# Kernel optimization log

Hardware: AMD Instinct MI355X
Metric: run time of the kernel (lower is better)

Reference implementation:

```python
import jax, jax.numpy as jnp
import numpy as np

N_STEPS = 5
STATE_DIM = 512
ANN_DIM = 256
N_NODES = 2048
N_EDGE_TYPES = 4


def setup_inputs() -> dict:
    key = jax.random.key(0)
    ks = jax.random.split(key, 12)
    D, E, N = STATE_DIM, N_EDGE_TYPES, N_NODES
    s = 0.02
    adjacency = (jax.random.uniform(ks[0], (N, N * 2 * E)) < 0.015).astype(jnp.float32)
    annotations = jax.random.normal(ks[1], (N, ANN_DIM), dtype=jnp.float32)
    W_prop = jax.random.normal(ks[2], (2 * E, D, D), dtype=jnp.float32) * s
    b_prop = jnp.zeros((2 * E, D), dtype=jnp.float32)
    Wz = jax.random.normal(ks[3], (D, D), dtype=jnp.float32) * s
    Uz = jax.random.normal(ks[4], (D, D), dtype=jnp.float32) * s
    bz = jnp.zeros((D,), dtype=jnp.float32)
    Wr = jax.random.normal(ks[5], (D, D), dtype=jnp.float32) * s
    Ur = jax.random.normal(ks[6], (D, D), dtype=jnp.float32) * s
    br = jnp.zeros((D,), dtype=jnp.float32)
    Wh = jax.random.normal(ks[7], (D, D), dtype=jnp.float32) * s
    Uh = jax.random.normal(ks[8], (D, D), dtype=jnp.float32) * s
    bh = jnp.zeros((D,), dtype=jnp.float32)
    return dict(adjacency=adjacency, annotations=annotations, W_prop=W_prop, b_prop=b_prop,
                Wz=Wz, Uz=Uz, bz=bz, Wr=Wr, Ur=Ur, br=br, Wh=Wh, Uh=Uh, bh=bh)


def reference(adjacency, annotations, W_prop, b_prop, Wz, Uz, bz, Wr, Ur, br, Wh, Uh, bh):
    N = annotations.shape[0]
    D = W_prop.shape[-1]
    # pad annotations into first columns of state (input1[:, :ann_dim] = annotations)
    h = jnp.zeros((N, D), dtype=annotations.dtype).at[:, :annotations.shape[1]].set(annotations)
    for _ in range(N_STEPS):
        # per-edge-type linear transforms: edge_type_list [2E, N, D]
        t = jnp.einsum('nd,edf->enf', h, W_prop) + b_prop[:, None, :]
        # adjacency aggregation: A is [N, N*2E] with per-edge-type column blocks
        a = adjacency @ t.reshape(-1, D)  # [N, D]
        # GRU node update (UpdateNet)
        z = jax.nn.sigmoid(a @ Wz + h @ Uz + bz)
        r = jax.nn.sigmoid(a @ Wr + h @ Ur + br)
        h_tilde = jnp.tanh(a @ Wh + (r * h) @ Uh + bh)
        h = (1.0 - z) * h + z * h_tilde
    return h
```

## Files before the change

### kernel.cpp

```cpp
#include <hip/hip_runtime.h>

typedef __attribute__((ext_vector_type(8))) short short8;
typedef __attribute__((ext_vector_type(4))) float floatx4;
typedef __attribute__((ext_vector_type(2))) unsigned uintx2;

#define NSTEPS 5
#define DD 512
#define ANN 256
#define NNODE 2048
#define NEDGE 8
#define NCOLS (NNODE * NEDGE)
#define MAXE 96
#define KP (NEDGE * DD)


typedef __attribute__((address_space(3))) unsigned lds_u32;
typedef const __attribute__((address_space(1))) unsigned g_u32;
__device__ __forceinline__ void gload16(const short* g, short* l) {
    __builtin_amdgcn_global_load_lds((g_u32*)g, (lds_u32*)l, 16, 0, 0);
}

__device__ inline float bf2f(unsigned short s) {
    unsigned u = ((unsigned)s) << 16;
    float f; __builtin_memcpy(&f, &u, 4);
    return f;
}
__device__ inline unsigned short f2bf(float f) {
    unsigned u; __builtin_memcpy(&u, &f, 4);
    u += 0x7fffu + ((u >> 16) & 1u);
    return (unsigned short)(u >> 16);
}
__device__ inline void split2(float x, unsigned short& hi, unsigned short& lo) {
    hi = f2bf(x);
    lo = f2bf(x - bf2f(hi));
}
__device__ inline void fo_write(short* __restrict__ Fhi, short* __restrict__ Flo,
                                int row, int col, float v) {
    unsigned short hs, ls;
    split2(v, hs, ls);
    size_t a = ((size_t)(row >> 4) * 64 + (col >> 3)) * 128 + ((row & 15) << 3) + (col & 7);
    Fhi[a] = (short)hs;
    Flo[a] = (short)ls;
}
__device__ inline void fo_write2(short* __restrict__ Fhi, short* __restrict__ Flo,
                                 int row, int c, float v0, float v1) {
    unsigned short h0, l0, h1, l1;
    split2(v0, h0, l0);
    split2(v1, h1, l1);
    size_t a = ((size_t)(row >> 4) * 64 + (c >> 3)) * 128 + ((row & 15) << 3) + (c & 7);
    *(unsigned*)(Fhi + a) = (unsigned)h0 | ((unsigned)h1 << 16);
    *(unsigned*)(Flo + a) = (unsigned)l0 | ((unsigned)l1 << 16);
}

__global__ __launch_bounds__(256) void k_init(const float* __restrict__ ann,
                                              float* __restrict__ h,
                                              short* __restrict__ HBhi,
                                              short* __restrict__ HBlo,
                                              int* __restrict__ cnt2,
                                              unsigned short* __restrict__ idx) {
    int n = blockIdx.x, t = threadIdx.x;
    int c = 2 * t;
    float v0 = 0.f, v1 = 0.f;
    if (c < ANN) {
        v0 = ann[(size_t)n * ANN + c];
        v1 = ann[(size_t)n * ANN + c + 1];
    }
    h[(size_t)n * DD + c]     = v0;
    h[(size_t)n * DD + c + 1] = v1;
    fo_write2(HBhi, HBlo, n, c, v0, v1);
    if (t < NEDGE) cnt2[n * NEDGE + t] = 0;
    unsigned* ip = (unsigned*)(idx + (size_t)n * NEDGE * MAXE);
    for (int j = t; j < NEDGE * MAXE / 2; j += 256)
        ip[j] = 2048u | (2048u << 16);
    if (n == 0) {
        h[(size_t)NNODE * DD + c]     = 0.f;
        h[(size_t)NNODE * DD + c + 1] = 0.f;
    }
}

__global__ __launch_bounds__(256) void k_build(const float* __restrict__ adj,
                                               int* __restrict__ cnt2,
                                               unsigned short* __restrict__ idx) {
    int n = blockIdx.x;
    const float* row = adj + (size_t)n * NCOLS;
    for (int j8 = threadIdx.x; j8 < NCOLS / 8; j8 += 256) {
        floatx4 a = *(const floatx4*)(row + j8 * 8);
        floatx4 b = *(const floatx4*)(row + j8 * 8 + 4);
        unsigned nz = 0;
        #pragma unroll
        for (int i = 0; i < 4; i++) {
            if (a[i] != 0.f) nz |= 1u << i;
            if (b[i] != 0.f) nz |= 1u << (4 + i);
        }
        while (nz) {
            int i = __builtin_ctz(nz);
            nz &= nz - 1;
            int j = j8 * 8 + i;
            int e = j >> 11;
            int m = j & (NNODE - 1);
            int p = atomicAdd(&cnt2[n * NEDGE + e], 1);
            if (p < MAXE) idx[((size_t)n * NEDGE + e) * MAXE + p] = (unsigned short)m;
        }
    }
}

__global__ __launch_bounds__(256) void k_transP(const float* __restrict__ W,
                                                short* __restrict__ Fhi,
                                                short* __restrict__ Flo, int K) {
    __shared__ float st[32][33];
    int tx = threadIdx.x & 31, ty = threadIdx.x >> 5;
    int k0 = blockIdx.x * 32, n0 = blockIdx.y * 32;
    #pragma unroll
    for (int i = 0; i < 4; i++)
        st[ty + i * 8][tx] = W[(size_t)(k0 + ty + i * 8) * DD + n0 + tx];
    __syncthreads();
    #pragma unroll
    for (int i = 0; i < 4; i++) {
        int n = n0 + ty + i * 8, k = k0 + tx;
        float v = st[tx][ty + i * 8];
        unsigned short hs, ls;
        split2(v, hs, ls);
        size_t a = ((size_t)(n >> 4) * (K >> 3) + (k >> 3)) * 128 + ((n & 15) << 3) + (k & 7);
        Fhi[a] = (short)hs;
        Flo[a] = (short)ls;
    }
}

__global__ __launch_bounds__(256) void k_transG(const float* __restrict__ s00,
                                                const float* __restrict__ s10,
                                                const float* __restrict__ s01,
                                                const float* __restrict__ s11,
                                                short* __restrict__ Fhi,
                                                short* __restrict__ Flo) {
    __shared__ float st[32][33];
    const int K = 2 * DD;
    int tx = threadIdx.x & 31, ty = threadIdx.x >> 5;
    int k0 = blockIdx.x * 32, n0 = blockIdx.y * 32;
    const float* sk0 = (n0 < DD) ? s00 : s01;
    const float* sk1 = (n0 < DD) ? s10 : s11;
    #pragma unroll
    for (int i = 0; i < 4; i++) {
        int k = k0 + ty + i * 8;
        const float* s = (k < DD) ? sk0 : sk1;
        st[ty + i * 8][tx] = s[(size_t)(k & (DD - 1)) * DD + ((n0 + tx) & (DD - 1))];
    }
    __syncthreads();
    #pragma unroll
    for (int i = 0; i < 4; i++) {
        int n = n0 + ty + i * 8, k = k0 + tx;
        float v = st[tx][ty + i * 8];
        unsigned short hs, ls;
        split2(v, hs, ls);
        size_t a = ((size_t)(n >> 4) * (K >> 3) + (k >> 3)) * 128 + ((n & 15) << 3) + (k & 7);
        Fhi[a] = (short)hs;
        Flo[a] = (short)ls;
    }
}

__global__ __launch_bounds__(256) void k_gather_all(const float* __restrict__ h,
                                                    const int* __restrict__ cnt2,
                                                    const unsigned short* __restrict__ idx,
                                                    short* __restrict__ Gbhi,
                                                    short* __restrict__ Gblo) {
    __shared__ unsigned short sidx[8 * MAXE];
    __shared__ int scnt[8];
    const int bid = blockIdx.x;
    const int ep = bid & 3;
    const int g  = bid >> 2;
    const int n0 = g * 4;
    const int t  = threadIdx.x;
    const int dn = t >> 6;
    const int th2 = t & 63;

    if (t < 8) scnt[t] = cnt2[(n0 + (t >> 1)) * NEDGE + 2 * ep + (t & 1)];
    {
        const unsigned* src0 = (const unsigned*)(idx + ((size_t)n0 * NEDGE + 2 * ep) * MAXE);
        for (int j = t; j < 384; j += 256) {
            int d = j / 96;
            int w = j - d * 96;
            ((unsigned*)sidx)[d * 96 + w] = src0[(size_t)d * (NEDGE * MAXE / 2) + w];
        }
    }
    __syncthreads();

    const float* hp = h + 8 * th2;

    floatx4 e0c0, e0c1, e1c0, e1c1;
    auto gather_edge = [&](int le, floatx4& o0, floatx4& o1) {
        int m = scnt[dn * 2 + le];
        m = m > MAXE ? MAXE : m;
        m = (m + 3) & ~3;
        const unsigned short* row = &sidx[dn * 192 + le * 96];
        floatx4 a0 = (floatx4){0.f, 0.f, 0.f, 0.f};
        floatx4 a1 = (floatx4){0.f, 0.f, 0.f, 0.f};
        floatx4 b0 = (floatx4){0.f, 0.f, 0.f, 0.f};
        floatx4 b1 = (floatx4){0.f, 0.f, 0.f, 0.f};
        for (int i = 0; i < m; i += 4) {
            uintx2 w = *(const uintx2*)(row + i);
            const float* r0 = hp + (size_t)(w[0] & 0xffffu) * DD;
            const float* r1 = hp + (size_t)(w[0] >> 16) * DD;
            const float* r2 = hp + (size_t)(w[1] & 0xffffu) * DD;
            const float* r3 = hp + (size_t)(w[1] >> 16) * DD;
            floatx4 v0 = *(const floatx4*)r0;
            floatx4 v1 = *(const floatx4*)(r0 + 4);
            floatx4 v2 = *(const floatx4*)r1;
            floatx4 v3 = *(const floatx4*)(r1 + 4);
            floatx4 v4 = *(const floatx4*)r2;
            floatx4 v5 = *(const floatx4*)(r2 + 4);
            floatx4 v6 = *(const floatx4*)r3;
            floatx4 v7 = *(const floatx4*)(r3 + 4);
            a0 += v0; a1 += v1; b0 += v2; b1 += v3;
            a0 += v4; a1 += v5; b0 += v6; b1 += v7;
        }
        o0 = a0 + b0;
        o1 = a1 + b1;
    };
    gather_edge(0, e0c0, e0c1);
    gather_edge(1, e1c0, e1c1);

    __syncthreads();

    #pragma unroll
    for (int le = 0; le < 2; le++) {
        floatx4 c0 = le ? e1c0 : e0c0;
        floatx4 c1 = le ? e1c1 : e0c1;
        int ge = 2 * ep + le;
        unsigned short hs[8], ls[8];
        #pragma unroll
        for (int j = 0; j < 4; j++) {
            split2(c0[j], hs[j], ls[j]);
            split2(c1[j], hs[4 + j], ls[4 + j]);
        }
        short8 hv, lv;
        #pragma unroll
        for (int j = 0; j < 8; j++) { hv[j] = (short)hs[j]; lv[j] = (short)ls[j]; }
        size_t a = ((size_t)(n0 >> 4) * 512 + ge * 64 + th2) * 128
                 + (size_t)((n0 & 15) + dn) * 8;
        *(short8*)(Gbhi + a) = hv;
        *(short8*)(Gblo + a) = lv;
    }
}

template<int MODE>
__global__ __launch_bounds__(256, 4) void k_gemm8(
    const short* __restrict__ A0hi, const short* __restrict__ A0lo,
    const short* __restrict__ A1hi, const short* __restrict__ A1lo,
    const short* __restrict__ Bhi,  const short* __restrict__ Blo,
    const float* __restrict__ bias0, const float* __restrict__ bias1,
    float* __restrict__ zbuf,
    float* __restrict__ h,
    short* __restrict__ Ohi, short* __restrict__ Olo,
    float* __restrict__ P0, float* __restrict__ P1) {

    __shared__ short S[24][512];

    const int tid = threadIdx.x;
    const int lane = tid & 63;
    const int wave = tid >> 6;
    const int wm = wave >> 1;
    const int wn = wave & 1;
    const int quad = lane >> 4;
    const int l16 = lane & 15;

    const int pbid = blockIdx.x;
    const int x = pbid & 7;
    const int j = pbid >> 3;
    const int mband = x * 4 + (j & 3);
    int kh, bx;
    if (MODE == 1) { kh = 0; bx = j >> 2; }
    else           { kh = (j >> 2) & 1; bx = j >> 3; }
    const int blockM = mband * 64;
    const int blockN = bx * 32;
    const int mt0 = blockM >> 4, nt0 = blockN >> 4;
    const int KCB = (MODE == 0) ? 512 : 128;
    const int bko = (MODE == 0) ? kh * 256 : (MODE == 2 ? kh * 64 : 0);
    const int Kloc = (MODE == 0) ? 2048 : (MODE == 1 ? 1024 : 512);

    const short* Ahi_s = (MODE == 2 && kh) ? A1hi : A0hi;
    const short* Alo_s = (MODE == 2 && kh) ? A1lo : A0lo;

    floatx4 acc[2];
    acc[0] = (floatx4){0.f, 0.f, 0.f, 0.f};
    acc[1] = (floatx4){0.f, 0.f, 0.f, 0.f};

    auto gaddr = [&](int k0, int s) -> const short* {
        if (s < 16) {
            int pl = s >> 3, u = s & 7;
            int mt = u >> 1, ks = u & 1;
            const short* base;
            int kc, stride;
            if (MODE == 0) {
                base = pl ? A0lo : A0hi;
                kc = kh * 256 + (k0 >> 3) + ks * 4;
                stride = 512;
            } else if (MODE == 1) {
                int seg = k0 >> 9;
                base = seg ? (pl ? A1lo : A1hi) : (pl ? A0lo : A0hi);
                kc = ((k0 & 511) >> 3) + ks * 4;
                stride = 64;
            } else {
                base = pl ? Alo_s : Ahi_s;
                kc = (k0 >> 3) + ks * 4;
                stride = 64;
            }
            return base + ((size_t)(mt0 + mt) * stride + kc) * 128;
        } else {
            int u = s - 16, pl = u >> 2, ks = (u >> 1) & 1, nt = u & 1;
            const short* base = pl ? Blo : Bhi;
            return base + ((size_t)(nt0 + nt) * KCB + bko + (k0 >> 3) + ks * 4) * 128;
        }
    };

    for (int k0 = 0; k0 < Kloc; k0 += 64) {
        #pragma unroll
        for (int jj = 0; jj < 6; jj++) {
            int s = jj * 4 + wave;
            gload16(gaddr(k0, s) + lane * 8, &S[s][lane * 8]);
        }
        __syncthreads();

        #pragma unroll
        for (int ks = 0; ks < 2; ks++) {
            short8 ah[2], al[2], bh, bl;
            #pragma unroll
            for (int mi = 0; mi < 2; mi++) {
                ah[mi] = *(const short8*)&S[(wm * 2 + mi) * 2 + ks][lane * 8];
                al[mi] = *(const short8*)&S[8 + (wm * 2 + mi) * 2 + ks][lane * 8];
            }
            bh = *(const short8*)&S[16 + ks * 2 + wn][lane * 8];
            bl = *(const short8*)&S[20 + ks * 2 + wn][lane * 8];
            #pragma unroll
            for (int mi = 0; mi < 2; mi++) {
                acc[mi] = __builtin_amdgcn_mfma_f32_16x16x32_bf16(ah[mi], bh, acc[mi], 0, 0, 0);
                acc[mi] = __builtin_amdgcn_mfma_f32_16x16x32_bf16(ah[mi], bl, acc[mi], 0, 0, 0);
                acc[mi] = __builtin_amdgcn_mfma_f32_16x16x32_bf16(al[mi], bh, acc[mi], 0, 0, 0);
            }
        }
        __syncthreads();
    }

    float* P = kh ? P1 : P0;
    #pragma unroll
    for (int mi = 0; mi < 2; mi++) {
        int gcol = blockN + wn * 16 + l16;
        #pragma unroll
        for (int r = 0; r < 4; r++) {
            int grow = blockM + wm * 32 + mi * 16 + quad * 4 + r;
            float v = acc[mi][r];
            if (MODE == 0 || MODE == 2) {
                P[(size_t)grow * DD + gcol] = v;
            } else {
                if (gcol < DD) {
                    size_t o = (size_t)grow * DD + gcol;
                    zbuf[o] = 1.f / (1.f + __expf(-(v + bias0[gcol])));
                } else {
                    int c = gcol - DD;
                    size_t o = (size_t)grow * DD + c;
                    float rr = 1.f / (1.f + __expf(-(v + bias1[c])));
                    fo_write(Ohi, Olo, grow, c, rr * h[o]);
                }
            }
        }
    }
}

__global__ __launch_bounds__(256) void k_combP(const float* __restrict__ P0,
                                               const float* __restrict__ P1,
                                               const int* __restrict__ cnt2,
                                               const float* __restrict__ bp,
                                               short* __restrict__ Gahi,
                                               short* __restrict__ Galo) {
    int n = blockIdx.x, t = threadIdx.x;
    int c = 2 * t;
    float s0 = 0.f, s1 = 0.f;
    #pragma unroll
    for (int e = 0; e < NEDGE; e++) {
        float ce = (float)cnt2[n * NEDGE + e];
        s0 += ce * bp[e * DD + c];
        s1 += ce * bp[e * DD + c + 1];
    }
    size_t o = (size_t)n * DD + c;
    float v0 = P0[o] + P1[o] + s0;
    float v1 = P0[o + 1] + P1[o + 1] + s1;
    fo_write2(Gahi, Galo, n, c, v0, v1);
}

__global__ __launch_bounds__(256) void k_combF(const float* __restrict__ P0,
                                               const float* __restrict__ P1,
                                               const float* __restrict__ bh,
                                               const float* __restrict__ zbuf,
                                               float* __restrict__ h,
                                               short* __restrict__ HBhi,
                                               short* __restrict__ HBlo,
                                               float* __restrict__ outF) {
    int n = blockIdx.x, t = threadIdx.x;
    int c = 2 * t;
    size_t o = (size_t)n * DD + c;
    float hn0, hn1;
    {
        float v = P0[o] + P1[o] + bh[c];
        hn0 = (1.f - zbuf[o]) * h[o] + zbuf[o] * tanhf(v);
    }
    {
        float v = P0[o + 1] + P1[o + 1] + bh[c + 1];
        hn1 = (1.f - zbuf[o + 1]) * h[o + 1] + zbuf[o + 1] * tanhf(v);
    }
    h[o] = hn0;
    h[o + 1] = hn1;
    fo_write2(HBhi, HBlo, n, c, hn0, hn1);
    outF[o] = hn0;
    outF[o + 1] = hn1;
}

extern "C" void kernel_launch(void* const* d_in, const int* in_sizes, int n_in,
                              void* d_out, int out_size, void* d_ws, size_t ws_size,
                              hipStream_t stream) {
    const float* adj = (const float*)d_in[0];
    const float* ann = (const float*)d_in[1];
    const float* Wp  = (const float*)d_in[2];
    const float* bp  = (const float*)d_in[3];
    const float* Wz  = (const float*)d_in[4];
    const float* Uz  = (const float*)d_in[5];
    const float* bz  = (const float*)d_in[6];
    const float* Wr  = (const float*)d_in[7];
    const float* Ur  = (const float*)d_in[8];
    const float* br  = (const float*)d_in[9];
    const float* Wh  = (const float*)d_in[10];
    const float* Uh  = (const float*)d_in[11];
    const float* bh  = (const float*)d_in[12];

    char* p = (char*)d_ws;
    float* h     = (float*)p; p += (size_t)(NNODE + 1) * DD * 4;
    float* abuf  = (float*)p; p += (size_t)NNODE * DD * 4;
    float* P0    = (float*)p; p += (size_t)NNODE * DD * 4;
    float* P1    = (float*)p; p += (size_t)NNODE * DD * 4;
    short* Gbhi  = (short*)p; p += (size_t)NNODE * KP * 2;
    short* Gblo  = (short*)p; p += (size_t)NNODE * KP * 2;
    short* Gahi  = (short*)p; p += (size_t)NNODE * DD * 2;
    short* Galo  = (short*)p; p += (size_t)NNODE * DD * 2;
    short* HBhi  = (short*)p; p += (size_t)NNODE * DD * 2;
    short* HBlo  = (short*)p; p += (size_t)NNODE * DD * 2;
    short* RHhi  = (short*)p; p += (size_t)NNODE * DD * 2;
    short* RHlo  = (short*)p; p += (size_t)NNODE * DD * 2;
    short* WpThi = (short*)p; p += (size_t)DD * KP * 2;
    short* WpTlo = (short*)p; p += (size_t)DD * KP * 2;
    short* ZRhi  = (short*)p; p += (size_t)(2 * DD) * (2 * DD) * 2;
    short* ZRlo  = (short*)p; p += (size_t)(2 * DD) * (2 * DD) * 2;
    short* HThi  = (short*)p; p += (size_t)DD * (2 * DD) * 2;
    short* HTlo  = (short*)p; p += (size_t)DD * (2 * DD) * 2;
    unsigned short* idx = (unsigned short*)p;
    p += (size_t)NNODE * NEDGE * MAXE * 2;
    int* cnt2 = (int*)p; p += (size_t)NNODE * NEDGE * 4;

    float* outF = (float*)d_out;

    k_init<<<NNODE, 256, 0, stream>>>(ann, h, HBhi, HBlo, cnt2, idx);
    k_build<<<NNODE, 256, 0, stream>>>(adj, cnt2, idx);
    k_transP<<<dim3(KP / 32, DD / 32), 256, 0, stream>>>(Wp, WpThi, WpTlo, KP);
    k_transG<<<dim3(32, 32), 256, 0, stream>>>(Wz, Uz, Wr, Ur, ZRhi, ZRlo);
    k_transG<<<dim3(32, 16), 256, 0, stream>>>(Wh, Uh, Wh, Uh, HThi, HTlo);

    for (int s = 0; s < NSTEPS; s++) {
        k_gather_all<<<2048, 256, 0, stream>>>(h, cnt2, idx, Gbhi, Gblo);
        k_gemm8<0><<<1024, 256, 0, stream>>>(Gbhi, Gblo, nullptr, nullptr,
                                             WpThi, WpTlo, nullptr, nullptr,
                                             nullptr, nullptr, nullptr, nullptr, P0, P1);
        k_combP<<<NNODE, 256, 0, stream>>>(P0, P1, cnt2, bp, Gahi, Galo);
        k_gemm8<1><<<1024, 256, 0, stream>>>(Gahi, Galo, HBhi, HBlo,
                                             ZRhi, ZRlo, bz, br,
                                             abuf, h, RHhi, RHlo, nullptr, nullptr);
        k_gemm8<2><<<1024, 256, 0, stream>>>(Gahi, Galo, RHhi, RHlo,
                                             HThi, HTlo, nullptr, nullptr,
                                             nullptr, nullptr, nullptr, nullptr, P0, P1);
        k_combF<<<NNODE, 256, 0, stream>>>(P0, P1, bh, abuf, h, HBhi, HBlo, outF);
    }
}
```

Baseline: 906.8 us.

## Widen GEMM tiles to 64x64 and use four-way split-K for propagation GEMM

```diff
diff --git a/kernel.cpp b/kernel.cpp
--- a/kernel.cpp
+++ b/kernel.cpp
@@ -12,6 +12,7 @@
 #define NCOLS (NNODE * NEDGE)
 #define MAXE 96
 #define KP (NEDGE * DD)
+#define NND (NNODE * DD)
 
 
 typedef __attribute__((address_space(3))) unsigned lds_u32;
@@ -250,9 +251,9 @@
     float* __restrict__ zbuf,
     float* __restrict__ h,
     short* __restrict__ Ohi, short* __restrict__ Olo,
-    float* __restrict__ P0, float* __restrict__ P1) {
-
-    __shared__ short S[24][512];
+    float* __restrict__ Pb) {
+
+    __shared__ short S[32][512];
 
     const int tid = threadIdx.x;
     const int lane = tid & 63;
@@ -267,21 +268,25 @@
     const int j = pbid >> 3;
     const int mband = x * 4 + (j & 3);
     int kh, bx;
-    if (MODE == 1) { kh = 0; bx = j >> 2; }
-    else           { kh = (j >> 2) & 1; bx = j >> 3; }
+    if (MODE == 0)      { bx = (j >> 2) & 7; kh = j >> 5; }
+    else if (MODE == 1) { bx = j >> 2;       kh = 0;      }
+    else                { kh = (j >> 2) & 1; bx = j >> 3; }
     const int blockM = mband * 64;
-    const int blockN = bx * 32;
+    const int blockN = bx * 64;
     const int mt0 = blockM >> 4, nt0 = blockN >> 4;
     const int KCB = (MODE == 0) ? 512 : 128;
-    const int bko = (MODE == 0) ? kh * 256 : (MODE == 2 ? kh * 64 : 0);
-    const int Kloc = (MODE == 0) ? 2048 : (MODE == 1 ? 1024 : 512);
+    const int bko = (MODE == 0) ? kh * 128 : (MODE == 2 ? kh * 64 : 0);
+    const int Kloc = (MODE == 2) ? 512 : 1024;
 
     const short* Ahi_s = (MODE == 2 && kh) ? A1hi : A0hi;
     const short* Alo_s = (MODE == 2 && kh) ? A1lo : A0lo;
 
-    floatx4 acc[2];
-    acc[0] = (floatx4){0.f, 0.f, 0.f, 0.f};
-    acc[1] = (floatx4){0.f, 0.f, 0.f, 0.f};
+    floatx4 acc[2][2];
+    #pragma unroll
+    for (int mi = 0; mi < 2; mi++)
+        #pragma unroll
+        for (int ni = 0; ni < 2; ni++)
+            acc[mi][ni] = (floatx4){0.f, 0.f, 0.f, 0.f};
 
     auto gaddr = [&](int k0, int s) -> const short* {
         if (s < 16) {
@@ -291,7 +296,7 @@
             int kc, stride;
             if (MODE == 0) {
                 base = pl ? A0lo : A0hi;
-                kc = kh * 256 + (k0 >> 3) + ks * 4;
+                kc = kh * 128 + (k0 >> 3) + ks * 4;
                 stride = 512;
             } else if (MODE == 1) {
                 int seg = k0 >> 9;
@@ -305,7 +310,7 @@
             }
             return base + ((size_t)(mt0 + mt) * stride + kc) * 128;
         } else {
-            int u = s - 16, pl = u >> 2, ks = (u >> 1) & 1, nt = u & 1;
+            int u = s - 16, pl = u >> 3, nt = (u & 7) >> 1, ks = u & 1;
             const short* base = pl ? Blo : Bhi;
             return base + ((size_t)(nt0 + nt) * KCB + bko + (k0 >> 3) + ks * 4) * 128;
         }
@@ -313,7 +318,7 @@
 
     for (int k0 = 0; k0 < Kloc; k0 += 64) {
         #pragma unroll
-        for (int jj = 0; jj < 6; jj++) {
+        for (int jj = 0; jj < 8; jj++) {
             int s = jj * 4 + wave;
             gload16(gaddr(k0, s) + lane * 8, &S[s][lane * 8]);
         }
@@ -321,51 +326,58 @@
 
         #pragma unroll
         for (int ks = 0; ks < 2; ks++) {
-            short8 ah[2], al[2], bh, bl;
+            short8 ah[2], al[2], bh[2], bl[2];
             #pragma unroll
             for (int mi = 0; mi < 2; mi++) {
                 ah[mi] = *(const short8*)&S[(wm * 2 + mi) * 2 + ks][lane * 8];
                 al[mi] = *(const short8*)&S[8 + (wm * 2 + mi) * 2 + ks][lane * 8];
             }
-            bh = *(const short8*)&S[16 + ks * 2 + wn][lane * 8];
-            bl = *(const short8*)&S[20 + ks * 2 + wn][lane * 8];
             #pragma unroll
-            for (int mi = 0; mi < 2; mi++) {
-                acc[mi] = __builtin_amdgcn_mfma_f32_16x16x32_bf16(ah[mi], bh, acc[mi], 0, 0, 0);
-                acc[mi] = __builtin_amdgcn_mfma_f32_16x16x32_bf16(ah[mi], bl, acc[mi], 0, 0, 0);
-                acc[mi] = __builtin_amdgcn_mfma_f32_16x16x32_bf16(al[mi], bh, acc[mi], 0, 0, 0);
+            for (int ni = 0; ni < 2; ni++) {
+                bh[ni] = *(const short8*)&S[16 + (wn * 2 + ni) * 2 + ks][lane * 8];
+                bl[ni] = *(const short8*)&S[24 + (wn * 2 + ni) * 2 + ks][lane * 8];
             }
+            #pragma unroll
+            for (int mi = 0; mi < 2; mi++)
+                #pragma unroll
+                for (int ni = 0; ni < 2; ni++) {
+                    acc[mi][ni] = __builtin_amdgcn_mfma_f32_16x16x32_bf16(ah[mi], bh[ni], acc[mi][ni], 0, 0, 0);
+                    acc[mi][ni] = __builtin_amdgcn_mfma_f32_16x16x32_bf16(ah[mi], bl[ni], acc[mi][ni], 0, 0, 0);
+                    acc[mi][ni] = __builtin_amdgcn_mfma_f32_16x16x32_bf16(al[mi], bh[ni], acc[mi][ni], 0, 0, 0);
+                }
         }
         __syncthreads();
     }
 
-    float* P = kh ? P1 : P0;
+    float* P = Pb + (size_t)kh * NND;
     #pragma unroll
     for (int mi = 0; mi < 2; mi++) {
-        int gcol = blockN + wn * 16 + l16;
-        #pragma unroll
-        for (int r = 0; r < 4; r++) {
-            int grow = blockM + wm * 32 + mi * 16 + quad * 4 + r;
-            float v = acc[mi][r];
-            if (MODE == 0 || MODE == 2) {
-                P[(size_t)grow * DD + gcol] = v;
-            } else {
-                if (gcol < DD) {
-                    size_t o = (size_t)grow * DD + gcol;
-                    zbuf[o] = 1.f / (1.f + __expf(-(v + bias0[gcol])));
+        #pragma unroll
+        for (int ni = 0; ni < 2; ni++) {
+            int gcol = blockN + wn * 32 + ni * 16 + l16;
+            #pragma unroll
+            for (int r = 0; r < 4; r++) {
+                int grow = blockM + wm * 32 + mi * 16 + quad * 4 + r;
+                float v = acc[mi][ni][r];
+                if (MODE == 0 || MODE == 2) {
+                    P[(size_t)grow * DD + gcol] = v;
                 } else {
-                    int c = gcol - DD;
-                    size_t o = (size_t)grow * DD + c;
-                    float rr = 1.f / (1.f + __expf(-(v + bias1[c])));
-                    fo_write(Ohi, Olo, grow, c, rr * h[o]);
+                    if (gcol < DD) {
+                        size_t o = (size_t)grow * DD + gcol;
+                        zbuf[o] = 1.f / (1.f + __expf(-(v + bias0[gcol])));
+                    } else {
+                        int c = gcol - DD;
+                        size_t o = (size_t)grow * DD + c;
+                        float rr = 1.f / (1.f + __expf(-(v + bias1[c])));
+                        fo_write(Ohi, Olo, grow, c, rr * h[o]);
+                    }
                 }
             }
         }
     }
 }
 
-__global__ __launch_bounds__(256) void k_combP(const float* __restrict__ P0,
-                                               const float* __restrict__ P1,
+__global__ __launch_bounds__(256) void k_combP(const float* __restrict__ Pb,
                                                const int* __restrict__ cnt2,
                                                const float* __restrict__ bp,
                                                short* __restrict__ Gahi,
@@ -380,13 +392,16 @@
         s1 += ce * bp[e * DD + c + 1];
     }
     size_t o = (size_t)n * DD + c;
-    float v0 = P0[o] + P1[o] + s0;
-    float v1 = P0[o + 1] + P1[o + 1] + s1;
+    float v0 = s0, v1 = s1;
+    #pragma unroll
+    for (int kh = 0; kh < 4; kh++) {
+        v0 += Pb[o + (size_t)kh * NND];
+        v1 += Pb[o + 1 + (size_t)kh * NND];
+    }
     fo_write2(Gahi, Galo, n, c, v0, v1);
 }
 
-__global__ __launch_bounds__(256) void k_combF(const float* __restrict__ P0,
-                                               const float* __restrict__ P1,
+__global__ __launch_bounds__(256) void k_combF(const float* __restrict__ Pb,
                                                const float* __restrict__ bh,
                                                const float* __restrict__ zbuf,
                                                float* __restrict__ h,
@@ -398,11 +413,11 @@
     size_t o = (size_t)n * DD + c;
     float hn0, hn1;
     {
-        float v = P0[o] + P1[o] + bh[c];
+        float v = Pb[o] + Pb[o + NND] + bh[c];
         hn0 = (1.f - zbuf[o]) * h[o] + zbuf[o] * tanhf(v);
     }
     {
-        float v = P0[o + 1] + P1[o + 1] + bh[c + 1];
+        float v = Pb[o + 1] + Pb[o + 1 + NND] + bh[c + 1];
         hn1 = (1.f - zbuf[o + 1]) * h[o + 1] + zbuf[o + 1] * tanhf(v);
     }
     h[o] = hn0;
@@ -432,8 +447,7 @@
     char* p = (char*)d_ws;
     float* h     = (float*)p; p += (size_t)(NNODE + 1) * DD * 4;
     float* abuf  = (float*)p; p += (size_t)NNODE * DD * 4;
-    float* P0    = (float*)p; p += (size_t)NNODE * DD * 4;
-    float* P1    = (float*)p; p += (size_t)NNODE * DD * 4;
+    float* Pb    = (float*)p; p += (size_t)4 * NND * 4;
     short* Gbhi  = (short*)p; p += (size_t)NNODE * KP * 2;
     short* Gblo  = (short*)p; p += (size_t)NNODE * KP * 2;
     short* Gahi  = (short*)p; p += (size_t)NNODE * DD * 2;
@@ -464,14 +478,14 @@
         k_gather_all<<<2048, 256, 0, stream>>>(h, cnt2, idx, Gbhi, Gblo);
         k_gemm8<0><<<1024, 256, 0, stream>>>(Gbhi, Gblo, nullptr, nullptr,
                                              WpThi, WpTlo, nullptr, nullptr,
-                                             nullptr, nullptr, nullptr, nullptr, P0, P1);
-        k_combP<<<NNODE, 256, 0, stream>>>(P0, P1, cnt2, bp, Gahi, Galo);
-        k_gemm8<1><<<1024, 256, 0, stream>>>(Gahi, Galo, HBhi, HBlo,
-                                             ZRhi, ZRlo, bz, br,
-                                             abuf, h, RHhi, RHlo, nullptr, nullptr);
-        k_gemm8<2><<<1024, 256, 0, stream>>>(Gahi, Galo, RHhi, RHlo,
-                                             HThi, HTlo, nullptr, nullptr,
-                                             nullptr, nullptr, nullptr, nullptr, P0, P1);
-        k_combF<<<NNODE, 256, 0, stream>>>(P0, P1, bh, abuf, h, HBhi, HBlo, outF);
-    }
-}
+                                             nullptr, nullptr, nullptr, nullptr, Pb);
+        k_combP<<<NNODE, 256, 0, stream>>>(Pb, cnt2, bp, Gahi, Galo);
+        k_gemm8<1><<<512, 256, 0, stream>>>(Gahi, Galo, HBhi, HBlo,
+                                            ZRhi, ZRlo, bz, br,
+                                            abuf, h, RHhi, RHlo, nullptr);
+        k_gemm8<2><<<512, 256, 0, stream>>>(Gahi, Galo, RHhi, RHlo,
+                                            HThi, HTlo, nullptr, nullptr,
+                                            nullptr, nullptr, nullptr, nullptr, Pb);
+        k_combF<<<NNODE, 256, 0, stream>>>(Pb, bh, abuf, h, HBhi, HBlo, outF);
+    }
+}
```

Result: slower. 1.122 ms (+23.8%).
